# Kernel optimization log

Hardware: AMD Instinct MI355X
Metric: run time of the kernel (lower is better)

## Reference

```python
import jax, jax.numpy as jnp
import numpy as np

N_NODES = 20000
N_EDGES = 320000
N_GRAPHS = 200
N_LAYERS = 2
TOWERS = 5
F_IN = 75        # divide_input=False -> each tower sees the full 75-dim input
F_OUT = 15       # out_channels // towers = 75 // 5
EDGE_DIM = 50
POST_IN = (4 * 3 + 1) * F_IN  # 4 aggregators * 3 scalers + self = 975
EPS_STD = 1e-5
EPS_BN = 1e-5


def setup_inputs() -> dict:
    key = jax.random.key(0)
    ks = jax.random.split(key, 16)
    x_idx = jax.random.randint(ks[0], (N_NODES,), 0, 10000)
    edge_index = jax.random.randint(ks[1], (2, N_EDGES), 0, N_NODES)
    edge_attr_idx = jax.random.randint(ks[2], (N_EDGES,), 0, 100)
    batch_idx = jnp.sort(jax.random.randint(ks[3], (N_NODES,), 0, N_GRAPHS))

    def g(k, shp, fan):
        return jax.random.normal(k, shp, jnp.float32) * np.float32(1.0 / np.sqrt(fan))

    inp = dict(
        x_idx=x_idx, edge_index=edge_index, edge_attr_idx=edge_attr_idx, batch_idx=batch_idx,
        node_emb=g(ks[4], (10000, F_IN), 1.0),
        edge_emb=g(ks[5], (100, EDGE_DIM), 1.0),
        W_edge=g(ks[6], (N_LAYERS, EDGE_DIM, F_IN), EDGE_DIM),
        b_edge=jnp.zeros((N_LAYERS, F_IN), jnp.float32),
        W_pre=g(ks[7], (N_LAYERS, TOWERS, 3 * F_IN, F_IN), 3 * F_IN),
        b_pre=jnp.zeros((N_LAYERS, TOWERS, F_IN), jnp.float32),
        W_post=g(ks[8], (N_LAYERS, TOWERS, POST_IN, F_OUT), POST_IN),
        b_post=jnp.zeros((N_LAYERS, TOWERS, F_OUT), jnp.float32),
        W_lin=g(ks[9], (N_LAYERS, F_IN, F_IN), F_IN),
        b_lin=jnp.zeros((N_LAYERS, F_IN), jnp.float32),
        bn_gamma=jnp.ones((N_LAYERS, F_IN), jnp.float32),
        bn_beta=jnp.zeros((N_LAYERS, F_IN), jnp.float32),
        W1=g(ks[10], (75, 50), 75), b1=jnp.zeros((50,), jnp.float32),
        W2=g(ks[11], (50, 25), 50), b2=jnp.zeros((25,), jnp.float32),
        W3=g(ks[12], (25, 1), 25), b3=jnp.zeros((1,), jnp.float32),
    )
    return inp


def reference(x_idx, edge_index, edge_attr_idx, batch_idx,
              node_emb, edge_emb, W_edge, b_edge, W_pre, b_pre,
              W_post, b_post, W_lin, b_lin, bn_gamma, bn_beta,
              W1, b1, W2, b2, W3, b3):
    src, dst = edge_index[0], edge_index[1]  # flow source_to_target: aggregate at dst
    x = node_emb[x_idx]                      # [N, 75]
    e_raw = edge_emb[edge_attr_idx]          # [E, 50]

    # in-degree based scalers (PNA); avg log-degree from this graph's degree histogram
    deg = jax.ops.segment_sum(jnp.ones((N_EDGES,), jnp.float32), dst, num_segments=N_NODES)
    avg_log = jnp.mean(jnp.log(deg + 1.0))
    deg_c = jnp.maximum(deg, 1.0)
    amp = (jnp.log(deg_c + 1.0) / avg_log)[:, None, None]
    att = (avg_log / jnp.log(deg_c + 1.0))[:, None, None]
    has_in = (deg > 0.0)[:, None, None]
    inv_deg = (1.0 / deg_c)[:, None, None]

    for l in range(N_LAYERS):
        # edge encoder (shared across towers)
        e = e_raw @ W_edge[l] + b_edge[l]                            # [E, 75]
        # message: since divide_input=False all towers see the same concat input
        h = jnp.concatenate([x[dst], x[src], e], axis=-1)            # [E, 225]
        m = jnp.einsum('ec,tcf->etf', h, W_pre[l]) + b_pre[l]        # [E, T, 75]
        # multi-aggregator reduction at dst
        mean = jax.ops.segment_sum(m, dst, num_segments=N_NODES) * inv_deg
        mean_sq = jax.ops.segment_sum(m * m, dst, num_segments=N_NODES) * inv_deg
        std = jnp.sqrt(jax.nn.relu(mean_sq - mean * mean) + EPS_STD)
        mn = jnp.where(has_in, jax.ops.segment_min(m, dst, num_segments=N_NODES), 0.0)
        mx = jnp.where(has_in, jax.ops.segment_max(m, dst, num_segments=N_NODES), 0.0)
        aggr = jnp.concatenate([mean, mn, mx, std], axis=-1)         # [N, T, 300]
        # degree scalers: identity, amplification, attenuation
        out = jnp.concatenate([aggr, aggr * amp, aggr * att], axis=-1)  # [N, T, 900]
        # update: concat self features, per-tower post MLP, then shared lin
        xt = jnp.broadcast_to(x[:, None, :], (N_NODES, TOWERS, F_IN))
        h2 = jnp.concatenate([xt, out], axis=-1)                     # [N, T, 975]
        y = jnp.einsum('ntc,tcf->ntf', h2, W_post[l]) + b_post[l]    # [N, T, 15]
        y = y.reshape(N_NODES, TOWERS * F_OUT) @ W_lin[l] + b_lin[l] # [N, 75]
        # BatchNorm (training-mode batch stats, biased variance) + ReLU
        mu = jnp.mean(y, axis=0)
        var = jnp.mean((y - mu) ** 2, axis=0)
        y = (y - mu) * jax.lax.rsqrt(var + EPS_BN) * bn_gamma[l] + bn_beta[l]
        x = jax.nn.relu(y)

    pooled = jax.ops.segment_sum(x, batch_idx, num_segments=N_GRAPHS)  # [G, 75]
    h = jax.nn.relu(pooled @ W1 + b1)
    h = jax.nn.relu(h @ W2 + b2)
    return h @ W3 + b3                                               # [G, 1]
```

## Files before the change

kernel.cpp:

```cpp
#include <hip/hip_runtime.h>
#include <hip/hip_bf16.h>
#include <math.h>

#define NN 20000
#define NE 320000
#define NG 200
#define FI 75
#define NT 5
#define FO 15
#define CH 375
#define PI 975
#define SMS 1608

typedef __attribute__((ext_vector_type(8))) short v8s;
typedef __attribute__((ext_vector_type(4))) float v4f;

__device__ __forceinline__ unsigned short f2bfu(float v) {
  __hip_bfloat16 h = __float2bfloat16(v);
  return *reinterpret_cast<unsigned short*>(&h);
}
__device__ __forceinline__ float uif(unsigned u) { return __uint_as_float(u); }

__global__ __launch_bounds__(256) void k_mega1(
    const int* __restrict__ xidx, const float* __restrict__ emb, float* __restrict__ x,
    const int* __restrict__ dstp, int* __restrict__ deg,
    const float* __restrict__ eemb, const float* __restrict__ W_edge,
    const float* __restrict__ b_edge, float* __restrict__ te,
    const float* __restrict__ W_pre, float* __restrict__ WAs,
    const float* __restrict__ W_post, float* __restrict__ V,
    const float* __restrict__ b_post, const float* __restrict__ W_lin,
    const float* __restrict__ b_lin, float* __restrict__ bc) {
  __shared__ float S[FI * 16];
  int b = blockIdx.x, tid = threadIdx.x;
  if (b < 5860) {
    int i = b * 256 + tid;
    if (i < NN * FI) {
      int n = i / FI, f = i - n * FI;
      x[i] = emb[xidx[n] * FI + f];
    }
  } else if (b < 7110) {
    int e = (b - 5860) * 256 + tid;
    if (e < NE) atomicAdd(&deg[dstp[e]], 1);
  } else if (b < 7310) {
    int la = b - 7110;
    int l = la / 100, a = la - l * 100;
    int f = tid;
    if (f < FI) {
      float acc = b_edge[l * FI + f];
      for (int j = 0; j < 50; ++j)
        acc = fmaf(eemb[a * 50 + j], W_edge[(l * 50 + j) * FI + f], acc);
      te[la * FI + f] = acc;
    }
  } else if (b < 7530) {
    int i = (b - 7310) * 256 + tid;
    if (i < 2 * FI * CH) {
      int c = i % CH;
      int k = (i / CH) % FI;
      int l = i / (CH * FI);
      int t = c / FI, f = c - t * FI;
      WAs[i] = W_pre[((size_t)(l * NT + t) * 225 + FI + k) * FI + f];
    }
  } else if (b < 7560) {
    int bid = b - 7530;
    int g = bid % 3;
    int lt = bid / 3;
    for (int idx = tid; idx < FI * 16; idx += 256) {
      int q = idx >> 4, f = idx & 15;
      float v = 0.f;
      if (f < FO) {
        const float* wb = W_post + (size_t)lt * PI * FO;
        int rowb = FI + g * 300 + q;
        v = wb[rowb * FO + f] + wb[(rowb + FI) * FO + f] + wb[(rowb + 2 * FI) * FO + f];
      }
      S[idx] = v;
    }
    __syncthreads();
    for (int idx = tid; idx < FI * 16; idx += 256) {
      int j = idx >> 4, f = idx & 15;
      float acc = 0.f;
      const float* wr = W_pre + ((size_t)lt * 225 + j) * FI;
      for (int q = 0; q < FI; ++q) acc = fmaf(wr[q], S[q * 16 + f], acc);
      V[((size_t)bid * FI + j) * 16 + f] = acc;
    }
  } else {
    int l = b - 7560;
    int g = tid;
    if (g < FI) {
      float acc = b_lin[l * FI + g];
      for (int j = 0; j < FI; ++j)
        acc = fmaf(b_post[l * FI + j], W_lin[(l * FI + j) * FI + g], acc);
      bc[l * 76 + g] = acc;
    }
  }
}

__global__ __launch_bounds__(1024) void k_mega2(
    const int* __restrict__ deg, int* __restrict__ off, int* __restrict__ cur,
    float* __restrict__ avglog,
    const float* __restrict__ te, const float* __restrict__ W_pre,
    const float* __restrict__ b_pre, unsigned short* __restrict__ tm,
    const float* __restrict__ W_post, const float* __restrict__ V,
    unsigned short* __restrict__ Bp,
    const float* __restrict__ WAs, unsigned short* __restrict__ Bxs,
    const float* __restrict__ W_lin, unsigned short* __restrict__ Blin) {
  __shared__ float red[1024];
  int b = blockIdx.x, t = threadIdx.x;
  if (b == 0) {
    int* wsum = (int*)red;
    int base = t * 20;
    int loc[20];
    int s = 0;
#pragma unroll
    for (int j = 0; j < 20; ++j) {
      int i = base + j;
      int v = (i < NN) ? deg[i] : 0;
      loc[j] = s;
      s += v;
    }
    int lane = t & 63, w = t >> 6;
    int inc = s;
    for (int o = 1; o < 64; o <<= 1) {
      int u = __shfl_up(inc, o, 64);
      if (lane >= o) inc += u;
    }
    if (lane == 63) wsum[w] = inc;
    __syncthreads();
    if (t == 0) {
      int a = 0;
#pragma unroll
      for (int k = 0; k < 16; ++k) { int v = wsum[k]; wsum[k] = a; a += v; }
    }
    __syncthreads();
    int tex = wsum[w] + inc - s;
#pragma unroll
    for (int j = 0; j < 20; ++j) {
      int i = base + j;
      if (i < NN) { int e = tex + loc[j]; off[i] = e; cur[i] = e; }
    }
    if (t == 1023) off[NN] = tex + s;
  } else if (b == 1) {
    float s = 0.f;
    for (int i = t; i < NN; i += 1024) s += logf((float)deg[i] + 1.f);
    red[t] = s;
    __syncthreads();
    for (int o = 512; o > 0; o >>= 1) {
      if (t < o) red[t] += red[t + o];
      __syncthreads();
    }
    if (t == 0) avglog[0] = red[0] / (float)NN;
  } else if (b < 77) {
    int idx = (b - 2) * 1024 + t;
    if (idx < 76800) {
      int la = idx / 384, c = idx - la * 384;
      int l = la / 100;
      float acc = 0.f;
      if (c < CH) {
        int tt = c / FI, f = c - tt * FI;
        acc = b_pre[(l * NT + tt) * FI + f];
        const float* ter = te + la * FI;
        for (int k = 0; k < FI; ++k)
          acc = fmaf(ter[k], W_pre[((size_t)(l * NT + tt) * 225 + 150 + k) * FI + f], acc);
      }
      tm[(size_t)la * 384 + c] = f2bfu(acc);
    }
  } else if (b < 302) {
    int i = (b - 77) * 1024 + t;
    if (i < 230400) {
      int j = i & 7;
      int lane = (i >> 3) & 63;
      int rem = i >> 9;
      int kb = rem % 15; rem /= 15;
      int g = rem % 3; rem /= 3;
      int tt = rem % 5;
      int l = rem / 5;
      int k = kb * 32 + (lane >> 4) * 8 + j;
      int f = lane & 15;
      float w = 0.f;
      if (f < FO) {
        int lt = l * NT + tt;
        if (k < 300) {
          int a = k / 75, ch = k - a * 75;
          w = W_post[((size_t)lt * PI + FI + g * 300 + a * 75 + ch) * FO + f];
        } else if (k >= 320 && k < 395) {
          w = V[(((size_t)(lt * 3 + g)) * FI + (k - 320)) * 16 + f];
        } else if (k >= 395 && k < 470 && g == 0) {
          w = W_post[((size_t)lt * PI + (k - 395)) * FO + f];
        }
      }
      Bp[i] = f2bfu(w);
    }
  } else if (b < 374) {
    int i = (b - 302) * 1024 + t;
    if (i < 73728) {
      int j = i & 7;
      int lane = (i >> 3) & 63;
      int rem = i >> 9;
      int nt = rem % 24; rem /= 24;
      int kb = rem % 3;
      int l = rem / 3;
      int k = kb * 32 + (lane >> 4) * 8 + j;
      int n = nt * 16 + (lane & 15);
      float w = 0.f;
      if (k < FI && n < CH) w = WAs[(size_t)l * FI * CH + k * CH + n];
      Bxs[i] = f2bfu(w);
    }
  } else {
    int i = (b - 374) * 1024 + t;
    if (i < 15360) {
      int j = i & 7;
      int lane = (i >> 3) & 63;
      int rem = i >> 9;
      int nt = rem % 5; rem /= 5;
      int kb = rem % 3;
      int l = rem / 3;
      int k = kb * 32 + (lane >> 4) * 8 + j;
      int f = nt * 16 + (lane & 15);
      float w = 0.f;
      if (k < FI && f < FI) w = W_lin[(size_t)l * FI * FI + k * FI + f];
      Blin[i] = f2bfu(w);
    }
  }
}

__global__ __launch_bounds__(256) void k_mega3(
    const int* __restrict__ srcp, const int* __restrict__ dstp,
    const int* __restrict__ attr, int* __restrict__ cur, int2* __restrict__ csr,
    const int* __restrict__ deg, const float* __restrict__ avglog,
    float* __restrict__ amp, float* __restrict__ att, float* __restrict__ inv) {
  int b = blockIdx.x, t = threadIdx.x;
  if (b < 1250) {
    int e = b * 256 + t;
    if (e < NE) {
      int pos = atomicAdd(&cur[dstp[e]], 1);
      csr[pos] = make_int2(srcp[e], attr[e]);
    }
  } else {
    int i = (b - 1250) * 256 + t;
    if (i < NN) {
      float dc = fmaxf((float)deg[i], 1.f);
      float ld = logf(dc + 1.f);
      float av = avglog[0];
      amp[i] = ld / av;
      att[i] = av / ld;
      inv[i] = 1.f / dc;
    }
  }
}

__global__ __launch_bounds__(256) void k_gemm_xs(const float* __restrict__ x,
                                                 const unsigned short* __restrict__ BxsL,
                                                 unsigned short* __restrict__ xsb,
                                                 const int* __restrict__ deg,
                                                 unsigned short* __restrict__ xh,
                                                 float* __restrict__ bnsum) {
  int tid = threadIdx.x;
  if (blockIdx.y == 1) {
    if (blockIdx.x == 0 && tid < 150) bnsum[tid] = 0.f;
    for (int i = blockIdx.x * 256 + tid; i < NN * 160; i += 625 * 256) {
      int r = i / 160, k = i - r * 160;
      float v = 0.f;
      if (k < FI) v = x[(size_t)r * FI + k] * ((deg[r] > 0) ? 1.f : 0.f);
      else if (k < 150) v = x[(size_t)r * FI + k - FI];
      xh[i] = f2bfu(v);
    }
    return;
  }
  __shared__ unsigned short As[32 * 104];
  __shared__ unsigned short Os[32 * 384];
  int m0 = blockIdx.x * 32;
  for (int i = tid; i < 32 * 104; i += 256) {
    int r = i / 104, k = i - r * 104;
    As[i] = (k < FI) ? f2bfu(x[(size_t)(m0 + r) * FI + k]) : 0;
  }
  __syncthreads();
  int lane = tid & 63, w = tid >> 6;
  int m16 = lane & 15, quad = lane >> 4;
  v4f acc0[6], acc1[6];
#pragma unroll
  for (int nt = 0; nt < 6; ++nt) {
    acc0[nt] = {0.f, 0.f, 0.f, 0.f};
    acc1[nt] = {0.f, 0.f, 0.f, 0.f};
  }
  const unsigned short* arow0 = As + m16 * 104 + quad * 8;
  const unsigned short* arow1 = As + (16 + m16) * 104 + quad * 8;
#pragma unroll
  for (int kb = 0; kb < 3; ++kb) {
    v8s a0 = *(const v8s*)(arow0 + kb * 32);
    v8s a1 = *(const v8s*)(arow1 + kb * 32);
#pragma unroll
    for (int nt = 0; nt < 6; ++nt) {
      v8s bf = *(const v8s*)(BxsL + ((size_t)(kb * 24 + w * 6 + nt) * 64 + lane) * 8);
      acc0[nt] = __builtin_amdgcn_mfma_f32_16x16x32_bf16(a0, bf, acc0[nt], 0, 0, 0);
      acc1[nt] = __builtin_amdgcn_mfma_f32_16x16x32_bf16(a1, bf, acc1[nt], 0, 0, 0);
    }
  }
#pragma unroll
  for (int nt = 0; nt < 6; ++nt) {
    int col = w * 96 + nt * 16 + m16;
#pragma unroll
    for (int r = 0; r < 4; ++r) {
      Os[(quad * 4 + r) * 384 + col] = f2bfu(acc0[nt][r]);
      Os[(16 + quad * 4 + r) * 384 + col] = f2bfu(acc1[nt][r]);
    }
  }
  __syncthreads();
  uint4* dst = (uint4*)(xsb + (size_t)m0 * 384);
  const uint4* src = (const uint4*)Os;
  for (int i = tid; i < 1536; i += 256) dst[i] = src[i];
}

__global__ __launch_bounds__(1024) void k_aggpost(
    const unsigned short* __restrict__ xs, const int2* __restrict__ csr,
    const int* __restrict__ off, const float* __restrict__ inv_deg,
    const unsigned short* __restrict__ tm, const unsigned short* __restrict__ xh,
    const unsigned short* __restrict__ Bp, const float* __restrict__ amp,
    const float* __restrict__ att, const unsigned short* __restrict__ BlinL,
    const float* __restrict__ bcL, float* __restrict__ yout,
    float* __restrict__ bnsum) {
  __shared__ __align__(16) unsigned short sm[16 * SMS];
  __shared__ __align__(16) unsigned short zs[16 * 96];
  __shared__ float ysum[FI], ysq[FI];
  int tid = threadIdx.x;
  int wv = tid >> 6, lane = tid & 63;
  int rel0 = blockIdx.x * 16;
  int n = rel0 + wv;
  if (tid < FI) { ysum[tid] = 0.f; ysq[tid] = 0.f; }
  for (int idx = tid; idx < 1600; idx += 1024) {
    int h = idx / 100, pp = idx - h * 100;
    int t = pp / 20, cc = pp - t * 20;
    sm[h * SMS + t * 320 + 300 + cc] = 0;
  }
  for (int i = tid; i < 16 * 21; i += 1024) {
    int r = i / 21, k = 75 + i - r * 21;
    zs[r * 96 + k] = 0;
  }
  if (n < NN) {
    int c0 = lane * 6;
    int o0 = off[n], o1 = off[n + 1];
    float s[6], q[6], mn[6], mx[6];
#pragma unroll
    for (int j = 0; j < 6; ++j) {
      s[j] = 0.f; q[j] = 0.f; mn[j] = INFINITY; mx[j] = -INFINITY;
    }
    auto proc = [&](uint3 xv, uint3 tv) {
      unsigned xa[3] = {xv.x, xv.y, xv.z};
      unsigned ta[3] = {tv.x, tv.y, tv.z};
#pragma unroll
      for (int j = 0; j < 3; ++j) {
        float z0 = uif(xa[j] << 16) + uif(ta[j] << 16);
        float z1 = uif(xa[j] & 0xffff0000u) + uif(ta[j] & 0xffff0000u);
        s[2 * j] += z0; q[2 * j] = fmaf(z0, z0, q[2 * j]);
        mn[2 * j] = fminf(mn[2 * j], z0); mx[2 * j] = fmaxf(mx[2 * j], z0);
        s[2 * j + 1] += z1; q[2 * j + 1] = fmaf(z1, z1, q[2 * j + 1]);
        mn[2 * j + 1] = fminf(mn[2 * j + 1], z1); mx[2 * j + 1] = fmaxf(mx[2 * j + 1], z1);
      }
    };
    int i = o0;
    for (; i + 4 <= o1; i += 4) {
      int2 e0 = csr[i], e1 = csr[i + 1], e2 = csr[i + 2], e3 = csr[i + 3];
      uint3 x0 = *(const uint3*)(xs + (size_t)e0.x * 384 + c0);
      uint3 t0 = *(const uint3*)(tm + (size_t)e0.y * 384 + c0);
      uint3 x1 = *(const uint3*)(xs + (size_t)e1.x * 384 + c0);
      uint3 t1 = *(const uint3*)(tm + (size_t)e1.y * 384 + c0);
      uint3 x2 = *(const uint3*)(xs + (size_t)e2.x * 384 + c0);
      uint3 t2 = *(const uint3*)(tm + (size_t)e2.y * 384 + c0);
      uint3 x3 = *(const uint3*)(xs + (size_t)e3.x * 384 + c0);
      uint3 t3 = *(const uint3*)(tm + (size_t)e3.y * 384 + c0);
      proc(x0, t0); proc(x1, t1); proc(x2, t2); proc(x3, t3);
    }
    for (; i < o1; ++i) {
      int2 e0 = csr[i];
      uint3 x0 = *(const uint3*)(xs + (size_t)e0.x * 384 + c0);
      uint3 t0 = *(const uint3*)(tm + (size_t)e0.y * 384 + c0);
      proc(x0, t0);
    }
    float inv = inv_deg[n];
    bool empty = (o1 == o0);
    unsigned short* srow = sm + wv * SMS;
#pragma unroll
    for (int j = 0; j < 6; ++j) {
      int c = c0 + j;
      if (c < CH) {
        float me = s[j] * inv;
        float sd = sqrtf(fmaxf(q[j] * inv - me * me, 0.f) + 1e-5f);
        float mnv = empty ? 0.f : mn[j];
        float mxv = empty ? 0.f : mx[j];
        int t = c / 75, ch = c - t * 75;
        unsigned short* bb = srow + t * 320;
        bb[ch] = f2bfu(me);
        bb[75 + ch] = f2bfu(mnv);
        bb[150 + ch] = f2bfu(mxv);
        bb[225 + ch] = f2bfu(sd);
      }
    }
  } else {
    uint* rowz = (uint*)(sm + wv * SMS);
    for (int idx2 = lane; idx2 < SMS / 2; idx2 += 64) rowz[idx2] = 0;
  }
  __syncthreads();
  int m16 = lane & 15, quad = lane >> 4;
  if (wv < NT) {
    int tw = wv;
    const unsigned short* arow = sm + m16 * SMS + tw * 320 + quad * 8;
    const unsigned short* xrow = xh + (size_t)(rel0 + m16) * 160 + quad * 8;
    const unsigned short* bp = Bp + ((size_t)tw * 3 * 15 * 64) * 8 + lane * 8;
    v4f a0 = {0.f, 0.f, 0.f, 0.f}, a1 = a0, a2 = a0;
#pragma unroll
    for (int kb = 0; kb < 15; ++kb) {
      v8s av = *(const v8s*)((kb < 10) ? (arow + kb * 32) : (xrow + (kb - 10) * 32));
      const unsigned short* bb = bp + (size_t)kb * 512;
      v8s b0 = *(const v8s*)(bb);
      v8s b1 = *(const v8s*)(bb + 15 * 512);
      v8s b2 = *(const v8s*)(bb + 30 * 512);
      a0 = __builtin_amdgcn_mfma_f32_16x16x32_bf16(av, b0, a0, 0, 0, 0);
      a1 = __builtin_amdgcn_mfma_f32_16x16x32_bf16(av, b1, a1, 0, 0, 0);
      a2 = __builtin_amdgcn_mfma_f32_16x16x32_bf16(av, b2, a2, 0, 0, 0);
    }
    int f = m16;
    if (f < FO) {
      int relZ = quad * 4;
#pragma unroll
      for (int r = 0; r < 4; ++r) {
        int nd = rel0 + relZ + r;
        int ndc = (nd < NN) ? nd : (NN - 1);
        float zz = a0[r] + amp[ndc] * a1[r] + att[ndc] * a2[r];
        zs[(relZ + r) * 96 + tw * FO + f] = f2bfu(zz);
      }
    }
  }
  __syncthreads();
  if (wv < NT) {
    int tw = wv;
    v4f acc2 = {0.f, 0.f, 0.f, 0.f};
#pragma unroll
    for (int kb = 0; kb < 3; ++kb) {
      v8s av = *(const v8s*)(zs + m16 * 96 + quad * 8 + kb * 32);
      v8s bl = *(const v8s*)(BlinL + ((size_t)(kb * 5 + tw) * 64 + lane) * 8);
      acc2 = __builtin_amdgcn_mfma_f32_16x16x32_bf16(av, bl, acc2, 0, 0, 0);
    }
    int fcol = tw * 16 + m16;
    if (fcol < FI) {
      float bcf = bcL[fcol];
      int nb = rel0 + quad * 4;
#pragma unroll
      for (int r = 0; r < 4; ++r) {
        int nd = nb + r;
        if (nd < NN) {
          float v = acc2[r] + bcf;
          yout[(size_t)nd * FI + fcol] = v;
          atomicAdd(&ysum[fcol], v);
          atomicAdd(&ysq[fcol], v * v);
        }
      }
    }
  }
  __syncthreads();
  if (tid < FI) {
    atomicAdd(&bnsum[tid], ysum[tid]);
    atomicAdd(&bnsum[FI + tid], ysq[tid]);
  }
}

__global__ __launch_bounds__(256) void k_bnfinapply(const float* __restrict__ y,
    const float* __restrict__ bnsum, const float* __restrict__ gamL,
    const float* __restrict__ betL, float* __restrict__ xo,
    const int* __restrict__ batch, float* __restrict__ pooled, int dopool) {
  __shared__ float sc[150];
  int tid = threadIdx.x;
  if (tid < FI) {
    float mu = bnsum[tid] / (float)NN;
    float var = bnsum[FI + tid] / (float)NN - mu * mu;
    float scl = gamL[tid] * rsqrtf(var + 1e-5f);
    sc[tid] = scl;
    sc[FI + tid] = betL[tid] - mu * scl;
  }
  if (!dopool) {
    for (int i = blockIdx.x * 256 + tid; i < NG * FI; i += gridDim.x * 256)
      pooled[i] = 0.f;
  }
  __syncthreads();
  int stride = gridDim.x * 256;
  for (int i = blockIdx.x * 256 + tid; i < NN * FI; i += stride) {
    int n = i / FI, f = i - n * FI;
    float v = fmaxf(fmaf(y[i], sc[f], sc[FI + f]), 0.f);
    xo[i] = v;
    if (dopool) atomicAdd(&pooled[batch[n] * FI + f], v);
  }
}

__global__ void k_head(const float* __restrict__ pooled, const float* __restrict__ W1,
                       const float* __restrict__ b1, const float* __restrict__ W2,
                       const float* __restrict__ b2, const float* __restrict__ W3,
                       const float* __restrict__ b3, float* __restrict__ out) {
  __shared__ float p[FI], h1[50], h2[25];
  int g = blockIdx.x, t = threadIdx.x;
  for (int i = t; i < FI; i += 64) p[i] = pooled[g * FI + i];
  __syncthreads();
  if (t < 50) {
    float a = b1[t];
    for (int j = 0; j < FI; ++j) a = fmaf(p[j], W1[j * 50 + t], a);
    h1[t] = fmaxf(a, 0.f);
  }
  __syncthreads();
  if (t < 25) {
    float a = b2[t];
    for (int j = 0; j < 50; ++j) a = fmaf(h1[j], W2[j * 25 + t], a);
    h2[t] = fmaxf(a, 0.f);
  }
  __syncthreads();
  if (t == 0) {
    float a = b3[0];
    for (int j = 0; j < 25; ++j) a = fmaf(h2[j], W3[j], a);
    out[g] = a;
  }
}

extern "C" void kernel_launch(void* const* d_in, const int* in_sizes, int n_in,
                              void* d_out, int out_size, void* d_ws, size_t ws_size,
                              hipStream_t stream) {
  const int* x_idx = (const int*)d_in[0];
  const int* eidx  = (const int*)d_in[1];
  const int* srcp  = eidx;
  const int* dstp  = eidx + NE;
  const int* eattr = (const int*)d_in[2];
  const int* batch = (const int*)d_in[3];
  const float* node_emb = (const float*)d_in[4];
  const float* edge_emb = (const float*)d_in[5];
  const float* W_edge = (const float*)d_in[6];
  const float* b_edge = (const float*)d_in[7];
  const float* W_pre  = (const float*)d_in[8];
  const float* b_pre  = (const float*)d_in[9];
  const float* W_post = (const float*)d_in[10];
  const float* b_post = (const float*)d_in[11];
  const float* W_lin  = (const float*)d_in[12];
  const float* b_lin  = (const float*)d_in[13];
  const float* gam = (const float*)d_in[14];
  const float* bet = (const float*)d_in[15];
  const float* W1 = (const float*)d_in[16];
  const float* b1 = (const float*)d_in[17];
  const float* W2 = (const float*)d_in[18];
  const float* b2 = (const float*)d_in[19];
  const float* W3 = (const float*)d_in[20];
  const float* b3 = (const float*)d_in[21];

  char* p = (char*)d_ws;
  auto alloc = [&](size_t b) -> char* {
    char* r = p;
    p += (b + 255) & ~(size_t)255;
    return r;
  };
  float* x_a   = (float*)alloc((size_t)NN * FI * 4);
  float* x_b   = (float*)alloc((size_t)NN * FI * 4);
  unsigned short* xs_bf = (unsigned short*)alloc((size_t)NN * 384 * 2);
  float* z     = (float*)alloc((size_t)NN * FI * 4);
  unsigned short* xh = (unsigned short*)alloc((size_t)(NN + 64) * 160 * 2);
  float* te    = (float*)alloc(2 * 100 * FI * 4);
  unsigned short* tm_bf = (unsigned short*)alloc((size_t)2 * 100 * 384 * 2);
  float* WAs   = (float*)alloc((size_t)2 * FI * CH * 4);
  float* V     = (float*)alloc((size_t)2 * NT * 3 * FI * 16 * 4);
  unsigned short* Bpk = (unsigned short*)alloc((size_t)230400 * 2);
  unsigned short* Bxs = (unsigned short*)alloc((size_t)73728 * 2);
  unsigned short* Blin = (unsigned short*)alloc((size_t)15360 * 2);
  float* bc    = (float*)alloc(2 * 76 * 4);
  float* ampv  = (float*)alloc((size_t)NN * 4);
  float* attv  = (float*)alloc((size_t)NN * 4);
  float* invv  = (float*)alloc((size_t)NN * 4);
  float* avglog = (float*)alloc(256);
  float* bnsum = (float*)alloc(2 * FI * 4);
  float* pooled = (float*)alloc((size_t)NG * FI * 4);
  int* deg = (int*)alloc((size_t)NN * 4);
  int* off = (int*)alloc((size_t)(NN + 1) * 4);
  int* cur = (int*)alloc((size_t)NN * 4);
  int2* csr = (int2*)alloc((size_t)NE * 8);

  hipMemsetAsync(deg, 0, (size_t)NN * 4, stream);

  k_mega1<<<7562, 256, 0, stream>>>(x_idx, node_emb, x_a, dstp, deg,
                                    edge_emb, W_edge, b_edge, te,
                                    W_pre, WAs, W_post, V,
                                    b_post, W_lin, b_lin, bc);
  k_mega2<<<389, 1024, 0, stream>>>(deg, off, cur, avglog,
                                    te, W_pre, b_pre, tm_bf, W_post, V, Bpk,
                                    WAs, Bxs, W_lin, Blin);
  k_mega3<<<1329, 256, 0, stream>>>(srcp, dstp, eattr, cur, csr,
                                    deg, avglog, ampv, attv, invv);

  for (int l = 0; l < 2; ++l) {
    const float* xin = (l == 0) ? x_a : x_b;
    float* xout = (l == 0) ? x_b : x_a;
    k_gemm_xs<<<dim3(625, 2), 256, 0, stream>>>(xin, Bxs + (size_t)l * 36864,
                                                xs_bf, deg, xh, bnsum);
    k_aggpost<<<1250, 1024, 0, stream>>>(xs_bf, csr, off, invv,
                                         tm_bf + (size_t)l * 100 * 384, xh,
                                         Bpk + (size_t)l * 115200, ampv, attv,
                                         Blin + (size_t)l * 7680, bc + l * 76,
                                         z, bnsum);
    k_bnfinapply<<<1250, 256, 0, stream>>>(z, bnsum, gam + l * FI, bet + l * FI,
                                           xout, batch, pooled, (l == 1) ? 1 : 0);
  }

  k_head<<<NG, 64, 0, stream>>>(pooled, W1, b1, W2, b2, W3, b3, (float*)d_out);
}
```

Before: 433.1 us.

## Sort nodes by in-degree so each aggregation block gets balanced wavefronts

Builds a degree histogram and a descending-degree permutation of nodes, then has the aggregation/post kernel process nodes in that order, so the 16 wavefronts in a block have similar edge counts. The xh staging buffer is written in permuted order to match, and outputs are scattered back through the permutation. This aims to cut idle time from load imbalance within a block. The cost is an extra histogram pass, a serial single-block bucket-placement pass, and scattered stores and gathers on amp/att and yout.

```diff
diff --git a/kernel.cpp b/kernel.cpp
--- a/kernel.cpp
+++ b/kernel.cpp
@@ -102,7 +102,8 @@
     const float* __restrict__ W_post, const float* __restrict__ V,
     unsigned short* __restrict__ Bp,
     const float* __restrict__ WAs, unsigned short* __restrict__ Bxs,
-    const float* __restrict__ W_lin, unsigned short* __restrict__ Blin) {
+    const float* __restrict__ W_lin, unsigned short* __restrict__ Blin,
+    int* __restrict__ hist) {
   __shared__ float red[1024];
   int b = blockIdx.x, t = threadIdx.x;
   if (b == 0) {
@@ -204,7 +205,7 @@
       if (k < FI && n < CH) w = WAs[(size_t)l * FI * CH + k * CH + n];
       Bxs[i] = f2bfu(w);
     }
-  } else {
+  } else if (b < 389) {
     int i = (b - 374) * 1024 + t;
     if (i < 15360) {
       int j = i & 7;
@@ -219,6 +220,18 @@
       if (k < FI && f < FI) w = W_lin[(size_t)l * FI * FI + k * FI + f];
       Blin[i] = f2bfu(w);
     }
+  } else {
+    int* lh = (int*)red;
+    if (t < 256) lh[t] = 0;
+    __syncthreads();
+    int i = (b - 389) * 1024 + t;
+    if (i < NN) {
+      int d = deg[i];
+      if (d > 255) d = 255;
+      atomicAdd(&lh[d], 1);
+    }
+    __syncthreads();
+    if (t < 256 && lh[t]) atomicAdd(&hist[t], lh[t]);
   }
 }
 
@@ -226,7 +239,9 @@
     const int* __restrict__ srcp, const int* __restrict__ dstp,
     const int* __restrict__ attr, int* __restrict__ cur, int2* __restrict__ csr,
     const int* __restrict__ deg, const float* __restrict__ avglog,
-    float* __restrict__ amp, float* __restrict__ att, float* __restrict__ inv) {
+    float* __restrict__ amp, float* __restrict__ att, float* __restrict__ inv,
+    const int* __restrict__ hist, int* __restrict__ perm) {
+  __shared__ int lb[256];
   int b = blockIdx.x, t = threadIdx.x;
   if (b < 1250) {
     int e = b * 256 + t;
@@ -234,7 +249,7 @@
       int pos = atomicAdd(&cur[dstp[e]], 1);
       csr[pos] = make_int2(srcp[e], attr[e]);
     }
-  } else {
+  } else if (b < 1329) {
     int i = (b - 1250) * 256 + t;
     if (i < NN) {
       float dc = fmaxf((float)deg[i], 1.f);
@@ -244,6 +259,20 @@
       att[i] = av / ld;
       inv[i] = 1.f / dc;
     }
+  } else {
+    if (t < 256) lb[t] = hist[t];
+    __syncthreads();
+    if (t == 0) {
+      int a = 0;
+      for (int d = 255; d >= 0; --d) { int v = lb[d]; lb[d] = a; a += v; }
+    }
+    __syncthreads();
+    for (int i = t; i < NN; i += 256) {
+      int d = deg[i];
+      if (d > 255) d = 255;
+      int pos = atomicAdd(&lb[d], 1);
+      perm[pos] = i;
+    }
   }
 }
 
@@ -252,15 +281,17 @@
                                                  unsigned short* __restrict__ xsb,
                                                  const int* __restrict__ deg,
                                                  unsigned short* __restrict__ xh,
-                                                 float* __restrict__ bnsum) {
+                                                 float* __restrict__ bnsum,
+                                                 const int* __restrict__ perm) {
   int tid = threadIdx.x;
   if (blockIdx.y == 1) {
     if (blockIdx.x == 0 && tid < 150) bnsum[tid] = 0.f;
     for (int i = blockIdx.x * 256 + tid; i < NN * 160; i += 625 * 256) {
       int r = i / 160, k = i - r * 160;
+      int node = perm[r];
       float v = 0.f;
-      if (k < FI) v = x[(size_t)r * FI + k] * ((deg[r] > 0) ? 1.f : 0.f);
-      else if (k < 150) v = x[(size_t)r * FI + k - FI];
+      if (k < FI) v = x[(size_t)node * FI + k] * ((deg[node] > 0) ? 1.f : 0.f);
+      else if (k < 150) v = x[(size_t)node * FI + k - FI];
       xh[i] = f2bfu(v);
     }
     return;
@@ -316,14 +347,15 @@
     const unsigned short* __restrict__ Bp, const float* __restrict__ amp,
     const float* __restrict__ att, const unsigned short* __restrict__ BlinL,
     const float* __restrict__ bcL, float* __restrict__ yout,
-    float* __restrict__ bnsum) {
+    float* __restrict__ bnsum, const int* __restrict__ perm) {
   __shared__ __align__(16) unsigned short sm[16 * SMS];
   __shared__ __align__(16) unsigned short zs[16 * 96];
   __shared__ float ysum[FI], ysq[FI];
+  __shared__ int pnode[16];
   int tid = threadIdx.x;
   int wv = tid >> 6, lane = tid & 63;
   int rel0 = blockIdx.x * 16;
-  int n = rel0 + wv;
+  if (tid < 16) pnode[tid] = perm[rel0 + tid];
   if (tid < FI) { ysum[tid] = 0.f; ysq[tid] = 0.f; }
   for (int idx = tid; idx < 1600; idx += 1024) {
     int h = idx / 100, pp = idx - h * 100;
@@ -334,7 +366,8 @@
     int r = i / 21, k = 75 + i - r * 21;
     zs[r * 96 + k] = 0;
   }
-  if (n < NN) {
+  {
+    int n = perm[rel0 + wv];
     int c0 = lane * 6;
     int o0 = off[n], o1 = off[n + 1];
     float s[6], q[6], mn[6], mx[6];
@@ -393,9 +426,6 @@
         bb[225 + ch] = f2bfu(sd);
       }
     }
-  } else {
-    uint* rowz = (uint*)(sm + wv * SMS);
-    for (int idx2 = lane; idx2 < SMS / 2; idx2 += 64) rowz[idx2] = 0;
   }
   __syncthreads();
   int m16 = lane & 15, quad = lane >> 4;
@@ -421,9 +451,8 @@
       int relZ = quad * 4;
 #pragma unroll
       for (int r = 0; r < 4; ++r) {
-        int nd = rel0 + relZ + r;
-        int ndc = (nd < NN) ? nd : (NN - 1);
-        float zz = a0[r] + amp[ndc] * a1[r] + att[ndc] * a2[r];
+        int nd = pnode[relZ + r];
+        float zz = a0[r] + amp[nd] * a1[r] + att[nd] * a2[r];
         zs[(relZ + r) * 96 + tw * FO + f] = f2bfu(zz);
       }
     }
@@ -441,16 +470,13 @@
     int fcol = tw * 16 + m16;
     if (fcol < FI) {
       float bcf = bcL[fcol];
-      int nb = rel0 + quad * 4;
 #pragma unroll
       for (int r = 0; r < 4; ++r) {
-        int nd = nb + r;
-        if (nd < NN) {
-          float v = acc2[r] + bcf;
-          yout[(size_t)nd * FI + fcol] = v;
-          atomicAdd(&ysum[fcol], v);
-          atomicAdd(&ysq[fcol], v * v);
-        }
+        int nd = pnode[quad * 4 + r];
+        float v = acc2[r] + bcf;
+        yout[(size_t)nd * FI + fcol] = v;
+        atomicAdd(&ysum[fcol], v);
+        atomicAdd(&ysq[fcol], v * v);
       }
     }
   }
@@ -572,29 +598,32 @@
   int* off = (int*)alloc((size_t)(NN + 1) * 4);
   int* cur = (int*)alloc((size_t)NN * 4);
   int2* csr = (int2*)alloc((size_t)NE * 8);
+  int* hist = (int*)alloc(256 * 4);
+  int* perm = (int*)alloc((size_t)NN * 4);
 
   hipMemsetAsync(deg, 0, (size_t)NN * 4, stream);
+  hipMemsetAsync(hist, 0, 256 * 4, stream);
 
   k_mega1<<<7562, 256, 0, stream>>>(x_idx, node_emb, x_a, dstp, deg,
                                     edge_emb, W_edge, b_edge, te,
                                     W_pre, WAs, W_post, V,
                                     b_post, W_lin, b_lin, bc);
-  k_mega2<<<389, 1024, 0, stream>>>(deg, off, cur, avglog,
+  k_mega2<<<409, 1024, 0, stream>>>(deg, off, cur, avglog,
                                     te, W_pre, b_pre, tm_bf, W_post, V, Bpk,
-                                    WAs, Bxs, W_lin, Blin);
-  k_mega3<<<1329, 256, 0, stream>>>(srcp, dstp, eattr, cur, csr,
-                                    deg, avglog, ampv, attv, invv);
+                                    WAs, Bxs, W_lin, Blin, hist);
+  k_mega3<<<1330, 256, 0, stream>>>(srcp, dstp, eattr, cur, csr,
+                                    deg, avglog, ampv, attv, invv, hist, perm);
 
   for (int l = 0; l < 2; ++l) {
     const float* xin = (l == 0) ? x_a : x_b;
     float* xout = (l == 0) ? x_b : x_a;
     k_gemm_xs<<<dim3(625, 2), 256, 0, stream>>>(xin, Bxs + (size_t)l * 36864,
-                                                xs_bf, deg, xh, bnsum);
+                                                xs_bf, deg, xh, bnsum, perm);
     k_aggpost<<<1250, 1024, 0, stream>>>(xs_bf, csr, off, invv,
                                          tm_bf + (size_t)l * 100 * 384, xh,
                                          Bpk + (size_t)l * 115200, ampv, attv,
                                          Blin + (size_t)l * 7680, bc + l * 76,
-                                         z, bnsum);
+                                         z, bnsum, perm);
     k_bnfinapply<<<1250, 256, 0, stream>>>(z, bnsum, gam + l * FI, bet + l * FI,
                                            xout, batch, pooled, (l == 1) ? 1 : 0);
   }
```

Measured after the change: 455.3 us. +5.1%, slower.

## Stage edge gathers through LDS with async global_load_lds ring buffer

Applied to the files above, without the earlier changes.

Replaces the per-edge direct global gathers in the aggregation loop with a per-wave 4-slot LDS ring filled by global_load_lds. Edge indices are loaded once per 64 edges and broadcast with readlane. The loop then keeps several row loads in flight with explicit vmcnt waits, aiming to hide gather latency. This adds about 96KB of LDS per block, which lowers occupancy. It also drops the n<NN guard and the zero-fill branch for out-of-range rows, which is only safe if NN divides evenly into the 16-row blocks.

```diff
diff --git a/kernel.cpp b/kernel.cpp
--- a/kernel.cpp
+++ b/kernel.cpp
@@ -20,6 +20,10 @@
   return *reinterpret_cast<unsigned short*>(&h);
 }
 __device__ __forceinline__ float uif(unsigned u) { return __uint_as_float(u); }
+
+#define GLD(gp, lp) __builtin_amdgcn_global_load_lds( \
+    (const __attribute__((address_space(1))) void*)(gp), \
+    (__attribute__((address_space(3))) void*)(lp), 16, 0, 0)
 
 __global__ __launch_bounds__(256) void k_mega1(
     const int* __restrict__ xidx, const float* __restrict__ emb, float* __restrict__ x,
@@ -318,12 +322,12 @@
     const float* __restrict__ bcL, float* __restrict__ yout,
     float* __restrict__ bnsum) {
   __shared__ __align__(16) unsigned short sm[16 * SMS];
+  __shared__ __align__(16) unsigned short rng[16 * 4 * 768];
   __shared__ __align__(16) unsigned short zs[16 * 96];
   __shared__ float ysum[FI], ysq[FI];
   int tid = threadIdx.x;
   int wv = tid >> 6, lane = tid & 63;
   int rel0 = blockIdx.x * 16;
-  int n = rel0 + wv;
   if (tid < FI) { ysum[tid] = 0.f; ysq[tid] = 0.f; }
   for (int idx = tid; idx < 1600; idx += 1024) {
     int h = idx / 100, pp = idx - h * 100;
@@ -334,7 +338,8 @@
     int r = i / 21, k = 75 + i - r * 21;
     zs[r * 96 + k] = 0;
   }
-  if (n < NN) {
+  {
+    int n = rel0 + wv;
     int c0 = lane * 6;
     int o0 = off[n], o1 = off[n + 1];
     float s[6], q[6], mn[6], mx[6];
@@ -355,24 +360,41 @@
         mn[2 * j + 1] = fminf(mn[2 * j + 1], z1); mx[2 * j + 1] = fmaxf(mx[2 * j + 1], z1);
       }
     };
-    int i = o0;
-    for (; i + 4 <= o1; i += 4) {
-      int2 e0 = csr[i], e1 = csr[i + 1], e2 = csr[i + 2], e3 = csr[i + 3];
-      uint3 x0 = *(const uint3*)(xs + (size_t)e0.x * 384 + c0);
-      uint3 t0 = *(const uint3*)(tm + (size_t)e0.y * 384 + c0);
-      uint3 x1 = *(const uint3*)(xs + (size_t)e1.x * 384 + c0);
-      uint3 t1 = *(const uint3*)(tm + (size_t)e1.y * 384 + c0);
-      uint3 x2 = *(const uint3*)(xs + (size_t)e2.x * 384 + c0);
-      uint3 t2 = *(const uint3*)(tm + (size_t)e2.y * 384 + c0);
-      uint3 x3 = *(const uint3*)(xs + (size_t)e3.x * 384 + c0);
-      uint3 t3 = *(const uint3*)(tm + (size_t)e3.y * 384 + c0);
-      proc(x0, t0); proc(x1, t1); proc(x2, t2); proc(x3, t3);
-    }
-    for (; i < o1; ++i) {
-      int2 e0 = csr[i];
-      uint3 x0 = *(const uint3*)(xs + (size_t)e0.x * 384 + c0);
-      uint3 t0 = *(const uint3*)(tm + (size_t)e0.y * 384 + c0);
-      proc(x0, t0);
+    unsigned short* rw = rng + wv * (4 * 768);
+    int lo16 = lane * 8;
+    for (int base = o0; base < o1; base += 64) {
+      int m = o1 - base; if (m > 64) m = 64;
+      int ecx = 0, ecy = 0;
+      if (base + lane < o1) {
+        int2 e = csr[base + lane];
+        ecx = e.x; ecy = e.y;
+      }
+      asm volatile("s_waitcnt vmcnt(0)" ::: "memory");
+      auto issue = [&](int j) {
+        int sv = __builtin_amdgcn_readlane(ecx, j);
+        int av = __builtin_amdgcn_readlane(ecy, j);
+        unsigned short* sl = rw + (j & 3) * 768;
+        if (lane < 48) {
+          GLD(xs + (size_t)sv * 384 + lo16, sl);
+          GLD(tm + (size_t)av * 384 + lo16, sl + 384);
+        }
+      };
+      auto consume = [&](int j) {
+        const unsigned short* sl = rw + (j & 3) * 768;
+        uint3 xv = *(const uint3*)(sl + c0);
+        uint3 tv = *(const uint3*)(sl + 384 + c0);
+        proc(xv, tv);
+      };
+      int pe = (m < 4) ? m : 4;
+      for (int j = 0; j < pe; ++j) issue(j);
+      for (int j = 4; j < m; ++j) {
+        asm volatile("s_waitcnt vmcnt(6)" ::: "memory");
+        consume(j - 4);
+        __builtin_amdgcn_sched_barrier(0);
+        issue(j);
+      }
+      asm volatile("s_waitcnt vmcnt(0)" ::: "memory");
+      for (int jj = (m > 4 ? m - 4 : 0); jj < m; ++jj) consume(jj);
     }
     float inv = inv_deg[n];
     bool empty = (o1 == o0);
@@ -393,9 +415,6 @@
         bb[225 + ch] = f2bfu(sd);
       }
     }
-  } else {
-    uint* rowz = (uint*)(sm + wv * SMS);
-    for (int idx2 = lane; idx2 < SMS / 2; idx2 += 64) rowz[idx2] = 0;
   }
   __syncthreads();
   int m16 = lane & 15, quad = lane >> 4;
```

Result: slower. 460.0 us (+6.2%).

## Recompute per-edge source projection with MFMA inside aggregation instead of gathering precomputed rows

Applied to the files above, without the earlier changes.

Drops the separate per-node GEMM that materialised 384-wide bf16 projected source features. The aggregation kernel now gathers 96-wide raw bf16 source features per edge into double-buffered shared tiles and runs the projection per edge with MFMA, adding the edge-type term from a shared-memory copy of the table. This trades more redundant MFMA work per edge (about 16x) and many block barriers in the edge loop for roughly 4x less gather traffic. It also adds about 77KB of LDS per block, which may lower occupancy.

```diff
diff --git a/kernel.cpp b/kernel.cpp
--- a/kernel.cpp
+++ b/kernel.cpp
@@ -247,83 +247,47 @@
   }
 }
 
-__global__ __launch_bounds__(256) void k_gemm_xs(const float* __restrict__ x,
-                                                 const unsigned short* __restrict__ BxsL,
-                                                 unsigned short* __restrict__ xsb,
-                                                 const int* __restrict__ deg,
-                                                 unsigned short* __restrict__ xh,
-                                                 float* __restrict__ bnsum) {
+__global__ __launch_bounds__(256) void k_prepx(const float* __restrict__ x,
+                                               const int* __restrict__ deg,
+                                               unsigned short* __restrict__ xh,
+                                               unsigned short* __restrict__ xq,
+                                               float* __restrict__ bnsum) {
   int tid = threadIdx.x;
-  if (blockIdx.y == 1) {
-    if (blockIdx.x == 0 && tid < 150) bnsum[tid] = 0.f;
-    for (int i = blockIdx.x * 256 + tid; i < NN * 160; i += 625 * 256) {
-      int r = i / 160, k = i - r * 160;
-      float v = 0.f;
-      if (k < FI) v = x[(size_t)r * FI + k] * ((deg[r] > 0) ? 1.f : 0.f);
-      else if (k < 150) v = x[(size_t)r * FI + k - FI];
-      xh[i] = f2bfu(v);
-    }
-    return;
-  }
-  __shared__ unsigned short As[32 * 104];
-  __shared__ unsigned short Os[32 * 384];
-  int m0 = blockIdx.x * 32;
-  for (int i = tid; i < 32 * 104; i += 256) {
-    int r = i / 104, k = i - r * 104;
-    As[i] = (k < FI) ? f2bfu(x[(size_t)(m0 + r) * FI + k]) : 0;
-  }
-  __syncthreads();
-  int lane = tid & 63, w = tid >> 6;
-  int m16 = lane & 15, quad = lane >> 4;
-  v4f acc0[6], acc1[6];
-#pragma unroll
-  for (int nt = 0; nt < 6; ++nt) {
-    acc0[nt] = {0.f, 0.f, 0.f, 0.f};
-    acc1[nt] = {0.f, 0.f, 0.f, 0.f};
-  }
-  const unsigned short* arow0 = As + m16 * 104 + quad * 8;
-  const unsigned short* arow1 = As + (16 + m16) * 104 + quad * 8;
-#pragma unroll
-  for (int kb = 0; kb < 3; ++kb) {
-    v8s a0 = *(const v8s*)(arow0 + kb * 32);
-    v8s a1 = *(const v8s*)(arow1 + kb * 32);
-#pragma unroll
-    for (int nt = 0; nt < 6; ++nt) {
-      v8s bf = *(const v8s*)(BxsL + ((size_t)(kb * 24 + w * 6 + nt) * 64 + lane) * 8);
-      acc0[nt] = __builtin_amdgcn_mfma_f32_16x16x32_bf16(a0, bf, acc0[nt], 0, 0, 0);
-      acc1[nt] = __builtin_amdgcn_mfma_f32_16x16x32_bf16(a1, bf, acc1[nt], 0, 0, 0);
-    }
-  }
-#pragma unroll
-  for (int nt = 0; nt < 6; ++nt) {
-    int col = w * 96 + nt * 16 + m16;
-#pragma unroll
-    for (int r = 0; r < 4; ++r) {
-      Os[(quad * 4 + r) * 384 + col] = f2bfu(acc0[nt][r]);
-      Os[(16 + quad * 4 + r) * 384 + col] = f2bfu(acc1[nt][r]);
-    }
-  }
-  __syncthreads();
-  uint4* dst = (uint4*)(xsb + (size_t)m0 * 384);
-  const uint4* src = (const uint4*)Os;
-  for (int i = tid; i < 1536; i += 256) dst[i] = src[i];
+  if (blockIdx.x == 0 && tid < 150) bnsum[tid] = 0.f;
+  for (int i = blockIdx.x * 256 + tid; i < NN * 160; i += 625 * 256) {
+    int r = i / 160, k = i - r * 160;
+    float v = 0.f;
+    if (k < FI) v = x[(size_t)r * FI + k] * ((deg[r] > 0) ? 1.f : 0.f);
+    else if (k < 150) v = x[(size_t)r * FI + k - FI];
+    xh[i] = f2bfu(v);
+  }
+  for (int i = blockIdx.x * 256 + tid; i < NN * 96; i += 625 * 256) {
+    int r = i / 96, k = i - r * 96;
+    xq[i] = (k < FI) ? f2bfu(x[(size_t)r * FI + k]) : 0;
+  }
 }
 
 __global__ __launch_bounds__(1024) void k_aggpost(
-    const unsigned short* __restrict__ xs, const int2* __restrict__ csr,
+    const unsigned short* __restrict__ xq, const int2* __restrict__ csr,
     const int* __restrict__ off, const float* __restrict__ inv_deg,
     const unsigned short* __restrict__ tm, const unsigned short* __restrict__ xh,
     const unsigned short* __restrict__ Bp, const float* __restrict__ amp,
     const float* __restrict__ att, const unsigned short* __restrict__ BlinL,
     const float* __restrict__ bcL, float* __restrict__ yout,
-    float* __restrict__ bnsum) {
+    float* __restrict__ bnsum, const unsigned short* __restrict__ BxsL) {
+  __shared__ __align__(16) unsigned short tml[100 * 384];
   __shared__ __align__(16) unsigned short sm[16 * SMS];
   __shared__ __align__(16) unsigned short zs[16 * 96];
+  __shared__ __align__(16) unsigned short As0[16 * 104];
+  __shared__ __align__(16) unsigned short As1[16 * 104];
+  __shared__ int offL[17];
+  __shared__ int cumT[17];
   __shared__ float ysum[FI], ysq[FI];
   int tid = threadIdx.x;
   int wv = tid >> 6, lane = tid & 63;
+  int m16 = lane & 15, quad = lane >> 4;
   int rel0 = blockIdx.x * 16;
-  int n = rel0 + wv;
+  if (tid < 17) offL[tid] = off[rel0 + tid];
   if (tid < FI) { ysum[tid] = 0.f; ysq[tid] = 0.f; }
   for (int idx = tid; idx < 1600; idx += 1024) {
     int h = idx / 100, pp = idx - h * 100;
@@ -334,71 +298,172 @@
     int r = i / 21, k = 75 + i - r * 21;
     zs[r * 96 + k] = 0;
   }
-  if (n < NN) {
-    int c0 = lane * 6;
-    int o0 = off[n], o1 = off[n + 1];
-    float s[6], q[6], mn[6], mx[6];
-#pragma unroll
-    for (int j = 0; j < 6; ++j) {
-      s[j] = 0.f; q[j] = 0.f; mn[j] = INFINITY; mx[j] = -INFINITY;
-    }
-    auto proc = [&](uint3 xv, uint3 tv) {
-      unsigned xa[3] = {xv.x, xv.y, xv.z};
-      unsigned ta[3] = {tv.x, tv.y, tv.z};
-#pragma unroll
-      for (int j = 0; j < 3; ++j) {
-        float z0 = uif(xa[j] << 16) + uif(ta[j] << 16);
-        float z1 = uif(xa[j] & 0xffff0000u) + uif(ta[j] & 0xffff0000u);
-        s[2 * j] += z0; q[2 * j] = fmaf(z0, z0, q[2 * j]);
-        mn[2 * j] = fminf(mn[2 * j], z0); mx[2 * j] = fmaxf(mx[2 * j], z0);
-        s[2 * j + 1] += z1; q[2 * j + 1] = fmaf(z1, z1, q[2 * j + 1]);
-        mn[2 * j + 1] = fminf(mn[2 * j + 1], z1); mx[2 * j + 1] = fmaxf(mx[2 * j + 1], z1);
+  {
+    const uint4* ts = (const uint4*)tm;
+    uint4* td = (uint4*)tml;
+    for (int i = tid; i < 4800; i += 1024) td[i] = ts[i];
+  }
+  __syncthreads();
+  if (tid == 0) {
+    int a = 0;
+#pragma unroll
+    for (int i = 0; i < 16; ++i) {
+      cumT[i] = a;
+      a += (offL[i + 1] - offL[i] + 15) >> 4;
+    }
+    cumT[16] = a;
+  }
+  int nt0 = (wv < 8) ? 2 * wv : 8 + wv;
+  v8s Bf00, Bf01, Bf02, Bf10, Bf11, Bf12;
+  Bf00 = *(const v8s*)(BxsL + ((size_t)(0 * 24 + nt0) * 64 + lane) * 8);
+  Bf01 = *(const v8s*)(BxsL + ((size_t)(1 * 24 + nt0) * 64 + lane) * 8);
+  Bf02 = *(const v8s*)(BxsL + ((size_t)(2 * 24 + nt0) * 64 + lane) * 8);
+  if (wv < 8) {
+    Bf10 = *(const v8s*)(BxsL + ((size_t)(0 * 24 + nt0 + 1) * 64 + lane) * 8);
+    Bf11 = *(const v8s*)(BxsL + ((size_t)(1 * 24 + nt0 + 1) * 64 + lane) * 8);
+    Bf12 = *(const v8s*)(BxsL + ((size_t)(2 * 24 + nt0 + 1) * 64 + lane) * 8);
+  } else { Bf10 = Bf00; Bf11 = Bf01; Bf12 = Bf02; }
+  {
+    float sd0 = sqrtf(1e-5f);
+    for (int i = 0; i < 16; ++i) {
+      if (offL[i + 1] == offL[i] && quad == 0) {
+#pragma unroll
+        for (int t2 = 0; t2 < 2; ++t2) {
+          if (t2 == 0 || wv < 8) {
+            int col = (nt0 + t2) * 16 + m16;
+            if (col < CH) {
+              int tcol = col / 75, ch = col - tcol * 75;
+              unsigned short* bb = sm + i * SMS + tcol * 320;
+              bb[ch] = 0; bb[75 + ch] = 0; bb[150 + ch] = 0; bb[225 + ch] = f2bfu(sd0);
+            }
+          }
+        }
       }
-    };
-    int i = o0;
-    for (; i + 4 <= o1; i += 4) {
-      int2 e0 = csr[i], e1 = csr[i + 1], e2 = csr[i + 2], e3 = csr[i + 3];
-      uint3 x0 = *(const uint3*)(xs + (size_t)e0.x * 384 + c0);
-      uint3 t0 = *(const uint3*)(tm + (size_t)e0.y * 384 + c0);
-      uint3 x1 = *(const uint3*)(xs + (size_t)e1.x * 384 + c0);
-      uint3 t1 = *(const uint3*)(tm + (size_t)e1.y * 384 + c0);
-      uint3 x2 = *(const uint3*)(xs + (size_t)e2.x * 384 + c0);
-      uint3 t2 = *(const uint3*)(tm + (size_t)e2.y * 384 + c0);
-      uint3 x3 = *(const uint3*)(xs + (size_t)e3.x * 384 + c0);
-      uint3 t3 = *(const uint3*)(tm + (size_t)e3.y * 384 + c0);
-      proc(x0, t0); proc(x1, t1); proc(x2, t2); proc(x3, t3);
-    }
-    for (; i < o1; ++i) {
-      int2 e0 = csr[i];
-      uint3 x0 = *(const uint3*)(xs + (size_t)e0.x * 384 + c0);
-      uint3 t0 = *(const uint3*)(tm + (size_t)e0.y * 384 + c0);
-      proc(x0, t0);
-    }
-    float inv = inv_deg[n];
-    bool empty = (o1 == o0);
-    unsigned short* srow = sm + wv * SMS;
-#pragma unroll
-    for (int j = 0; j < 6; ++j) {
-      int c = c0 + j;
-      if (c < CH) {
-        float me = s[j] * inv;
-        float sd = sqrtf(fmaxf(q[j] * inv - me * me, 0.f) + 1e-5f);
-        float mnv = empty ? 0.f : mn[j];
-        float mxv = empty ? 0.f : mx[j];
-        int t = c / 75, ch = c - t * 75;
-        unsigned short* bb = srow + t * 320;
-        bb[ch] = f2bfu(me);
-        bb[75 + ch] = f2bfu(mnv);
-        bb[150 + ch] = f2bfu(mxv);
-        bb[225 + ch] = f2bfu(sd);
+    }
+  }
+  __syncthreads();
+  float sA0 = 0.f, qA0 = 0.f, mnA0 = INFINITY, mxA0 = -INFINITY;
+  float sA1 = 0.f, qA1 = 0.f, mnA1 = INFINITY, mxA1 = -INFINITY;
+  int T = cumT[16];
+  int ci = 0, si = 0;
+  if (T > 0) {
+    while (0 >= cumT[si + 1]) ++si;
+    if (tid >= 832) {
+      int tid2 = tid - 832;
+      int base = offL[si];
+      int e = base + tid2 / 12;
+      int o1m1 = offL[si + 1] - 1;
+      if (e > o1m1) e = o1m1;
+      int c16 = tid2 % 12;
+      int2 ec = csr[e];
+      *(uint4*)&As0[(tid2 / 12) * 104 + c16 * 8] =
+          *(const uint4*)&xq[(size_t)ec.x * 96 + c16 * 8];
+    }
+  }
+  __syncthreads();
+  for (int t = 0; t < T; ++t) {
+    unsigned short* Acur = (t & 1) ? As1 : As0;
+    unsigned short* Anxt = (t & 1) ? As0 : As1;
+    uint4 sval;
+    bool doStage = (t + 1 < T) && (tid >= 832);
+    if (t + 1 < T) { while (t + 1 >= cumT[si + 1]) ++si; }
+    if (doStage) {
+      int tid2 = tid - 832;
+      int base = offL[si] + (t + 1 - cumT[si]) * 16;
+      int e = base + tid2 / 12;
+      int o1m1 = offL[si + 1] - 1;
+      if (e > o1m1) e = o1m1;
+      int2 ec = csr[e];
+      sval = *(const uint4*)&xq[(size_t)ec.x * 96 + (tid2 % 12) * 8];
+    }
+    while (t >= cumT[ci + 1]) ++ci;
+    int o0i = offL[ci], o1i = offL[ci + 1];
+    int base = o0i + (t - cumT[ci]) * 16;
+    int o1m1 = o1i - 1;
+    v8s av0 = *(const v8s*)(Acur + m16 * 104 + quad * 8);
+    v8s av1 = *(const v8s*)(Acur + m16 * 104 + 32 + quad * 8);
+    v8s av2 = *(const v8s*)(Acur + m16 * 104 + 64 + quad * 8);
+    int er = base + quad * 4;
+    int i0 = er, i1 = er + 1, i2 = er + 2, i3 = er + 3;
+    bool v0 = i0 <= o1m1, v1 = i1 <= o1m1, v2 = i2 <= o1m1, v3 = i3 <= o1m1;
+    if (i0 > o1m1) i0 = o1m1;
+    if (i1 > o1m1) i1 = o1m1;
+    if (i2 > o1m1) i2 = o1m1;
+    if (i3 > o1m1) i3 = o1m1;
+    int a0 = csr[i0].y, a1 = csr[i1].y, a2 = csr[i2].y, a3 = csr[i3].y;
+    {
+      v4f acc = {0.f, 0.f, 0.f, 0.f};
+      acc = __builtin_amdgcn_mfma_f32_16x16x32_bf16(av0, Bf00, acc, 0, 0, 0);
+      acc = __builtin_amdgcn_mfma_f32_16x16x32_bf16(av1, Bf01, acc, 0, 0, 0);
+      acc = __builtin_amdgcn_mfma_f32_16x16x32_bf16(av2, Bf02, acc, 0, 0, 0);
+      int col = nt0 * 16 + m16;
+      float z0 = acc[0] + uif((unsigned)tml[a0 * 384 + col] << 16);
+      float z1 = acc[1] + uif((unsigned)tml[a1 * 384 + col] << 16);
+      float z2 = acc[2] + uif((unsigned)tml[a2 * 384 + col] << 16);
+      float z3 = acc[3] + uif((unsigned)tml[a3 * 384 + col] << 16);
+      sA0 += (v0 ? z0 : 0.f) + (v1 ? z1 : 0.f) + (v2 ? z2 : 0.f) + (v3 ? z3 : 0.f);
+      qA0 = v0 ? fmaf(z0, z0, qA0) : qA0;  qA0 = v1 ? fmaf(z1, z1, qA0) : qA0;
+      qA0 = v2 ? fmaf(z2, z2, qA0) : qA0;  qA0 = v3 ? fmaf(z3, z3, qA0) : qA0;
+      mnA0 = v0 ? fminf(mnA0, z0) : mnA0;  mnA0 = v1 ? fminf(mnA0, z1) : mnA0;
+      mnA0 = v2 ? fminf(mnA0, z2) : mnA0;  mnA0 = v3 ? fminf(mnA0, z3) : mnA0;
+      mxA0 = v0 ? fmaxf(mxA0, z0) : mxA0;  mxA0 = v1 ? fmaxf(mxA0, z1) : mxA0;
+      mxA0 = v2 ? fmaxf(mxA0, z2) : mxA0;  mxA0 = v3 ? fmaxf(mxA0, z3) : mxA0;
+    }
+    if (wv < 8) {
+      v4f acc = {0.f, 0.f, 0.f, 0.f};
+      acc = __builtin_amdgcn_mfma_f32_16x16x32_bf16(av0, Bf10, acc, 0, 0, 0);
+      acc = __builtin_amdgcn_mfma_f32_16x16x32_bf16(av1, Bf11, acc, 0, 0, 0);
+      acc = __builtin_amdgcn_mfma_f32_16x16x32_bf16(av2, Bf12, acc, 0, 0, 0);
+      int col = (nt0 + 1) * 16 + m16;
+      float z0 = acc[0] + uif((unsigned)tml[a0 * 384 + col] << 16);
+      float z1 = acc[1] + uif((unsigned)tml[a1 * 384 + col] << 16);
+      float z2 = acc[2] + uif((unsigned)tml[a2 * 384 + col] << 16);
+      float z3 = acc[3] + uif((unsigned)tml[a3 * 384 + col] << 16);
+      sA1 += (v0 ? z0 : 0.f) + (v1 ? z1 : 0.f) + (v2 ? z2 : 0.f) + (v3 ? z3 : 0.f);
+      qA1 = v0 ? fmaf(z0, z0, qA1) : qA1;  qA1 = v1 ? fmaf(z1, z1, qA1) : qA1;
+      qA1 = v2 ? fmaf(z2, z2, qA1) : qA1;  qA1 = v3 ? fmaf(z3, z3, qA1) : qA1;
+      mnA1 = v0 ? fminf(mnA1, z0) : mnA1;  mnA1 = v1 ? fminf(mnA1, z1) : mnA1;
+      mnA1 = v2 ? fminf(mnA1, z2) : mnA1;  mnA1 = v3 ? fminf(mnA1, z3) : mnA1;
+      mxA1 = v0 ? fmaxf(mxA1, z0) : mxA1;  mxA1 = v1 ? fmaxf(mxA1, z1) : mxA1;
+      mxA1 = v2 ? fmaxf(mxA1, z2) : mxA1;  mxA1 = v3 ? fmaxf(mxA1, z3) : mxA1;
+    }
+    if (doStage) {
+      int tid2 = tid - 832;
+      *(uint4*)&Anxt[(tid2 / 12) * 104 + (tid2 % 12) * 8] = sval;
+    }
+    if (t == cumT[ci + 1] - 1) {
+      float inv = inv_deg[rel0 + ci];
+#pragma unroll
+      for (int t2 = 0; t2 < 2; ++t2) {
+        if (t2 == 1 && wv >= 8) break;
+        float S = (t2 == 0) ? sA0 : sA1;
+        float Q = (t2 == 0) ? qA0 : qA1;
+        float MN = (t2 == 0) ? mnA0 : mnA1;
+        float MX = (t2 == 0) ? mxA0 : mxA1;
+        S += __shfl_xor(S, 16); S += __shfl_xor(S, 32);
+        Q += __shfl_xor(Q, 16); Q += __shfl_xor(Q, 32);
+        MN = fminf(MN, __shfl_xor(MN, 16)); MN = fminf(MN, __shfl_xor(MN, 32));
+        MX = fmaxf(MX, __shfl_xor(MX, 16)); MX = fmaxf(MX, __shfl_xor(MX, 32));
+        if (quad == 0) {
+          int col = (nt0 + t2) * 16 + m16;
+          if (col < CH) {
+            float me = S * inv;
+            float sd = sqrtf(fmaxf(Q * inv - me * me, 0.f) + 1e-5f);
+            int tcol = col / 75, ch = col - tcol * 75;
+            unsigned short* bb = sm + ci * SMS + tcol * 320;
+            bb[ch] = f2bfu(me);
+            bb[75 + ch] = f2bfu(MN);
+            bb[150 + ch] = f2bfu(MX);
+            bb[225 + ch] = f2bfu(sd);
+          }
+        }
       }
-    }
-  } else {
-    uint* rowz = (uint*)(sm + wv * SMS);
-    for (int idx2 = lane; idx2 < SMS / 2; idx2 += 64) rowz[idx2] = 0;
-  }
-  __syncthreads();
-  int m16 = lane & 15, quad = lane >> 4;
+      sA0 = 0.f; qA0 = 0.f; mnA0 = INFINITY; mxA0 = -INFINITY;
+      sA1 = 0.f; qA1 = 0.f; mnA1 = INFINITY; mxA1 = -INFINITY;
+    }
+    __syncthreads();
+  }
+  __syncthreads();
   if (wv < NT) {
     int tw = wv;
     const unsigned short* arow = sm + m16 * SMS + tw * 320 + quad * 8;
@@ -551,7 +616,7 @@
   };
   float* x_a   = (float*)alloc((size_t)NN * FI * 4);
   float* x_b   = (float*)alloc((size_t)NN * FI * 4);
-  unsigned short* xs_bf = (unsigned short*)alloc((size_t)NN * 384 * 2);
+  unsigned short* xq = (unsigned short*)alloc((size_t)NN * 96 * 2);
   float* z     = (float*)alloc((size_t)NN * FI * 4);
   unsigned short* xh = (unsigned short*)alloc((size_t)(NN + 64) * 160 * 2);
   float* te    = (float*)alloc(2 * 100 * FI * 4);
@@ -588,13 +653,12 @@
   for (int l = 0; l < 2; ++l) {
     const float* xin = (l == 0) ? x_a : x_b;
     float* xout = (l == 0) ? x_b : x_a;
-    k_gemm_xs<<<dim3(625, 2), 256, 0, stream>>>(xin, Bxs + (size_t)l * 36864,
-                                                xs_bf, deg, xh, bnsum);
-    k_aggpost<<<1250, 1024, 0, stream>>>(xs_bf, csr, off, invv,
+    k_prepx<<<625, 256, 0, stream>>>(xin, deg, xh, xq, bnsum);
+    k_aggpost<<<1250, 1024, 0, stream>>>(xq, csr, off, invv,
                                          tm_bf + (size_t)l * 100 * 384, xh,
                                          Bpk + (size_t)l * 115200, ampv, attv,
                                          Blin + (size_t)l * 7680, bc + l * 76,
-                                         z, bnsum);
+                                         z, bnsum, Bxs + (size_t)l * 36864);
     k_bnfinapply<<<1250, 256, 0, stream>>>(z, bnsum, gam + l * FI, bet + l * FI,
                                            xout, batch, pooled, (l == 1) ? 1 : 0);
   }
```

Measured after the change: 733.6 us. +69.4%, slower.
